# Optimization experiments

Hardware: AMD Instinct MI355X
Metric: run time of the kernel (lower is better)

Reference implementation:

```python
import jax, jax.numpy as jnp
import numpy as np

N, E = 2048, 8192            # n_vertex, n_edge
HV, HE, MV, ME, P, Q = 256, 128, 256, 256, 3, 3
NEG = 1e6                    # PhysChem mask bias: veb = (vew - 1) * 1e6


def _leaky_relu(x, slope=0.01):
    return jnp.where(x >= 0, x, slope * x)


def setup_inputs() -> dict:
    key = jax.random.key(0)
    ks = jax.random.split(key, 12)
    # random graph: each edge has two distinct endpoints
    src = jax.random.randint(ks[0], (E,), 0, N)
    dst = (src + 1 + jax.random.randint(ks[1], (E,), 0, N - 1)) % N
    vew1 = jax.nn.one_hot(src, N, dtype=jnp.float32).T  # [N, E]
    vew2 = jax.nn.one_hot(dst, N, dtype=jnp.float32).T  # [N, E]
    veb1 = (vew1 - 1.0) * NEG
    veb2 = (vew2 - 1.0) * NEG
    s = lambda k, sh, fan: jax.random.normal(k, sh, jnp.float32) / np.sqrt(fan)
    return {
        "hv_ftr": jax.random.normal(ks[2], (N, HV), jnp.float32),
        "he_ftr": jax.random.normal(ks[3], (E, HE), jnp.float32),
        "p_ftr": jax.random.normal(ks[4], (N, P), jnp.float32),
        "q_ftr": jax.random.normal(ks[5], (N, Q), jnp.float32),
        "vew1": vew1, "vew2": vew2, "veb1": veb1, "veb2": veb2,
        "attend_w": s(ks[6], (HV, MV), HV),
        "attend_b": jnp.zeros((MV,), jnp.float32),
        "align_w": s(ks[7], (P + Q + HE, 1), P + Q + HE),
        "align_b": jnp.zeros((1,), jnp.float32),
        "link_w": s(ks[8], (HV + P + Q + HV, ME), HV + P + Q + HV),
        "link_b": jnp.zeros((ME,), jnp.float32),
    }


def reference(hv_ftr, he_ftr, p_ftr, q_ftr, vew1, vew2, veb1, veb2,
              attend_w, attend_b, align_w, align_b, link_w, link_b):
    vew_u = jnp.concatenate([vew1, vew2], axis=1)   # [N, 2E]
    vew_v = jnp.concatenate([vew2, vew1], axis=1)   # [N, 2E]
    veb_v = jnp.concatenate([veb2, veb1], axis=1)   # [N, 2E]

    hv_u = vew_u.T @ hv_ftr                          # [2E, HV]
    hv_v = vew_v.T @ hv_ftr                          # [2E, HV]
    p_uv = vew_v.T @ p_ftr - vew_u.T @ p_ftr         # [2E, P]
    q_uv = vew_v.T @ q_ftr - vew_u.T @ q_ftr         # [2E, Q]
    he2 = jnp.concatenate([he_ftr, he_ftr], axis=0)  # [2E, HE]

    attend = _leaky_relu(hv_v @ attend_w + attend_b)               # [2E, MV]
    align = jnp.concatenate([p_uv, q_uv, he2], axis=1) @ align_w + align_b  # [2E, 1]
    # vew_v @ diag(align) == vew_v * align broadcast over columns
    align_mat = vew_v * align[:, 0][None, :] + veb_v               # [N, 2E]
    soft = jax.nn.softmax(align_mat, axis=-1)
    mv_ftr = jax.nn.elu(soft @ attend)                             # [N, MV]

    me_in = jnp.concatenate([hv_u, p_uv, q_uv, hv_v], axis=1)      # [2E, 2HV+P+Q]
    me_ftr = _leaky_relu(me_in @ link_w + link_b)                  # [2E, ME]
    return (mv_ftr, me_ftr)
```

## Files before the change

### kernel.cpp

```cpp
#include <hip/hip_runtime.h>
#include <math.h>

#define N_V  2048
#define N_E  8192

#define NE4            (N_V * (N_E / 4))
#define SCAN_ITER      8
#define SCAN_BPM       (NE4 / (256 * SCAN_ITER))

static __device__ __forceinline__ float leaky(float x) {
    return x >= 0.f ? x : 0.01f * x;
}

static __device__ __forceinline__ void fma4(float4& c, float a, const float4& b) {
    c.x = fmaf(a, b.x, c.x);
    c.y = fmaf(a, b.y, c.y);
    c.z = fmaf(a, b.z, c.z);
    c.w = fmaf(a, b.w, c.w);
}

__global__ __launch_bounds__(256) void k_scan(const float4* __restrict__ vew1,
                                              const float4* __restrict__ vew2,
                                              int* __restrict__ src,
                                              int* __restrict__ dst)
{
    const int  bm     = blockIdx.x & (SCAN_BPM - 1);
    const bool second = blockIdx.x >= SCAN_BPM;
    const float4* __restrict__ p = second ? vew2 : vew1;
    int* __restrict__ arr        = second ? dst : src;

    const int base = bm * (256 * SCAN_ITER) + threadIdx.x;

    float4 v[SCAN_ITER];
#pragma unroll
    for (int k = 0; k < SCAN_ITER; ++k) v[k] = p[base + k * 256];

#pragma unroll
    for (int k = 0; k < SCAN_ITER; ++k) {
        const float4 q = v[k];
        if (q.x != 0.f || q.y != 0.f || q.z != 0.f || q.w != 0.f) {
            const int i  = base + k * 256;
            const int n  = i >> 11;
            const int e4 = (i & 2047) << 2;
            if (q.x != 0.f) arr[e4 + 0] = n;
            if (q.y != 0.f) arr[e4 + 1] = n;
            if (q.z != 0.f) arr[e4 + 2] = n;
            if (q.w != 0.f) arr[e4 + 3] = n;
        }
    }
}

__global__ __launch_bounds__(256) void k_indeg(const int* __restrict__ src,
                                               const int* __restrict__ dst,
                                               int* __restrict__ indeg)
{
    const int e = blockIdx.x * 256 + threadIdx.x;
    atomicAdd(&indeg[src[e]], 1);
    atomicAdd(&indeg[dst[e]], 1);
}

__global__ __launch_bounds__(256, 3) void k_gemm(const float* __restrict__ hv,
                                                 const float* __restrict__ attend_w,
                                                 const float* __restrict__ attend_b,
                                                 const float* __restrict__ link_w,
                                                 const float* __restrict__ link_b,
                                                 const float* __restrict__ p_ftr,
                                                 const float* __restrict__ q_ftr,
                                                 float* __restrict__ X,
                                                 float* __restrict__ Au,
                                                 float* __restrict__ Av,
                                                 float* __restrict__ mv_out)
{
    __shared__ float As[8 * 256];

    const int mat  = blockIdx.y;
    const int row0 = blockIdx.x * 8;
    const int tid  = threadIdx.x;

    {
        const float4* __restrict__ s4 = (const float4*)(hv + row0 * 256);
        float4* d4 = (float4*)As;
        d4[tid]       = s4[tid];
        d4[tid + 256] = s4[tid + 256];
    }
    __syncthreads();

    const int jq = tid & 63;
    const int rl = (tid >> 6) * 2;
    const float* __restrict__ Arow0 = As + rl * 256;
    const float* __restrict__ Arow1 = Arow0 + 256;
    const int r0 = row0 + rl;

    const float* __restrict__ B =
        (mat == 0) ? attend_w : (mat == 1 ? link_w : link_w + 262 * 256);
    const float4* __restrict__ B4 = (const float4*)B;

    float4 acc0 = make_float4(0.f, 0.f, 0.f, 0.f);
    float4 acc1 = make_float4(0.f, 0.f, 0.f, 0.f);

    float4 ba[8], bb[8];
#pragma unroll
    for (int t = 0; t < 8; ++t) ba[t] = B4[t * 64 + jq];

    for (int ks = 0; ks < 256; ks += 16) {
#pragma unroll
        for (int t = 0; t < 8; ++t) bb[t] = B4[(ks + 8 + t) * 64 + jq];
#pragma unroll
        for (int t4 = 0; t4 < 2; ++t4) {
            const float4 a0 = *reinterpret_cast<const float4*>(Arow0 + ks + t4 * 4);
            const float4 a1 = *reinterpret_cast<const float4*>(Arow1 + ks + t4 * 4);
            fma4(acc0, a0.x, ba[t4 * 4 + 0]);
            fma4(acc0, a0.y, ba[t4 * 4 + 1]);
            fma4(acc0, a0.z, ba[t4 * 4 + 2]);
            fma4(acc0, a0.w, ba[t4 * 4 + 3]);
            fma4(acc1, a1.x, ba[t4 * 4 + 0]);
            fma4(acc1, a1.y, ba[t4 * 4 + 1]);
            fma4(acc1, a1.z, ba[t4 * 4 + 2]);
            fma4(acc1, a1.w, ba[t4 * 4 + 3]);
        }
        const int kn = (ks + 16) & 255;
#pragma unroll
        for (int t = 0; t < 8; ++t) ba[t] = B4[(kn + t) * 64 + jq];
#pragma unroll
        for (int t4 = 0; t4 < 2; ++t4) {
            const float4 a0 = *reinterpret_cast<const float4*>(Arow0 + ks + 8 + t4 * 4);
            const float4 a1 = *reinterpret_cast<const float4*>(Arow1 + ks + 8 + t4 * 4);
            fma4(acc0, a0.x, bb[t4 * 4 + 0]);
            fma4(acc0, a0.y, bb[t4 * 4 + 1]);
            fma4(acc0, a0.z, bb[t4 * 4 + 2]);
            fma4(acc0, a0.w, bb[t4 * 4 + 3]);
            fma4(acc1, a1.x, bb[t4 * 4 + 0]);
            fma4(acc1, a1.y, bb[t4 * 4 + 1]);
            fma4(acc1, a1.z, bb[t4 * 4 + 2]);
            fma4(acc1, a1.w, bb[t4 * 4 + 3]);
        }
    }

    if (mat == 0) {
        const float4 bias = *reinterpret_cast<const float4*>(attend_b + jq * 4);
        float4 a[2] = {acc0, acc1};
#pragma unroll
        for (int r = 0; r < 2; ++r) {
            float4 x;
            x.x = leaky(a[r].x + bias.x);
            x.y = leaky(a[r].y + bias.y);
            x.z = leaky(a[r].z + bias.z);
            x.w = leaky(a[r].w + bias.w);
            *reinterpret_cast<float4*>(X + (r0 + r) * 256 + jq * 4) = x;
            float4 m;
            m.x = (x.x > 0.f) ? x.x : expm1f(x.x);
            m.y = (x.y > 0.f) ? x.y : expm1f(x.y);
            m.z = (x.z > 0.f) ? x.z : expm1f(x.z);
            m.w = (x.w > 0.f) ? x.w : expm1f(x.w);
            *reinterpret_cast<float4*>(mv_out + (r0 + r) * 256 + jq * 4) = m;
        }
    } else {
        float4 w6[6];
#pragma unroll
        for (int t = 0; t < 6; ++t)
            w6[t] = *reinterpret_cast<const float4*>(link_w + (256 + t) * 256 + jq * 4);
        float4 lb = make_float4(0.f, 0.f, 0.f, 0.f);
        if (mat == 2) lb = *reinterpret_cast<const float4*>(link_b + jq * 4);
        float4 a[2] = {acc0, acc1};
#pragma unroll
        for (int r = 0; r < 2; ++r) {
            const int row = r0 + r;
            float4 z = make_float4(0.f, 0.f, 0.f, 0.f);
#pragma unroll
            for (int t = 0; t < 3; ++t) {
                fma4(z, p_ftr[row * 3 + t], w6[t]);
                fma4(z, q_ftr[row * 3 + t], w6[3 + t]);
            }
            float4 o;
            if (mat == 1) {
                o.x = a[r].x - z.x; o.y = a[r].y - z.y;
                o.z = a[r].z - z.z; o.w = a[r].w - z.w;
                *reinterpret_cast<float4*>(Au + row * 256 + jq * 4) = o;
            } else {
                o.x = a[r].x + z.x + lb.x; o.y = a[r].y + z.y + lb.y;
                o.z = a[r].z + z.z + lb.z; o.w = a[r].w + z.w + lb.w;
                *reinterpret_cast<float4*>(Av + row * 256 + jq * 4) = o;
            }
        }
    }
}

__global__ __launch_bounds__(256) void k_sumall(const float* __restrict__ X,
                                                const int* __restrict__ indeg,
                                                float* __restrict__ sumAll)
{
    const int j  = threadIdx.x;
    const int m0 = blockIdx.x * 64;
    float s = 0.f;
    for (int m = m0; m < m0 + 64; ++m) {
        s = fmaf((float)indeg[m], X[m * 256 + j], s);
    }
    atomicAdd(&sumAll[j], s);
}

__global__ __launch_bounds__(256) void k_fix(const int* __restrict__ indeg,
                                             const float* __restrict__ sumAll,
                                             float* __restrict__ out)
{
    const int n = blockIdx.x;
    if (indeg[n] != 0) return;
    const float v = sumAll[threadIdx.x] * (1.0f / (2.0f * N_E));
    out[n * 256 + threadIdx.x] = (v > 0.f) ? v : expm1f(v);
}

__global__ __launch_bounds__(256) void k_me(const int* __restrict__ src,
                                            const int* __restrict__ dst,
                                            const float* __restrict__ Au,
                                            const float* __restrict__ Av,
                                            float* __restrict__ out_me)
{
    const int t    = threadIdx.x;
    const int lane = t & 63;
    const int e    = blockIdx.x * 4 + (t >> 6);
    int u, v;
    if (e < N_E) { u = src[e]; v = dst[e]; }
    else         { u = dst[e - N_E]; v = src[e - N_E]; }
    const float4 a = *reinterpret_cast<const float4*>(&Au[u * 256 + lane * 4]);
    const float4 b = *reinterpret_cast<const float4*>(&Av[v * 256 + lane * 4]);
    float4 o;
    o.x = leaky(a.x + b.x);
    o.y = leaky(a.y + b.y);
    o.z = leaky(a.z + b.z);
    o.w = leaky(a.w + b.w);
    *reinterpret_cast<float4*>(&out_me[e * 256 + lane * 4]) = o;
}

extern "C" void kernel_launch(void* const* d_in, const int* in_sizes, int n_in,
                              void* d_out, int out_size, void* d_ws, size_t ws_size,
                              hipStream_t stream) {
    const float* hv       = (const float*)d_in[0];
    const float* p_ftr    = (const float*)d_in[2];
    const float* q_ftr    = (const float*)d_in[3];
    const float* vew1     = (const float*)d_in[4];
    const float* vew2     = (const float*)d_in[5];
    const float* attend_w = (const float*)d_in[8];
    const float* attend_b = (const float*)d_in[9];
    const float* link_w   = (const float*)d_in[12];
    const float* link_b   = (const float*)d_in[13];

    float* out = (float*)d_out;
    float* ws  = (float*)d_ws;

    int*   src    = (int*)ws;
    int*   dst    = src + N_E;
    int*   indeg  = dst + N_E;
    float* sumAll = ws + 18432;
    float* X      = ws + 32768;
    float* Au     = X + N_V * 256;
    float* Av     = Au + N_V * 256;

    hipMemsetAsync(indeg, 0, (N_V + 256) * sizeof(int), stream);

    k_scan<<<2 * SCAN_BPM, 256, 0, stream>>>((const float4*)vew1,
                                             (const float4*)vew2, src, dst);

    k_indeg<<<N_E / 256, 256, 0, stream>>>(src, dst, indeg);

    dim3 g2(N_V / 8, 3);
    k_gemm<<<g2, 256, 0, stream>>>(hv, attend_w, attend_b, link_w, link_b,
                                   p_ftr, q_ftr, X, Au, Av, out);

    k_sumall<<<32, 256, 0, stream>>>(X, indeg, sumAll);

    k_fix<<<N_V, 256, 0, stream>>>(indeg, sumAll, out);

    k_me<<<(2 * N_E) / 4, 256, 0, stream>>>(src, dst, Au, Av, out + N_V * 256);
}
```

Before: 293.5 us.

## Fuse one-hot scan and dense GEMM into one interleaved launch

Merges the incidence-matrix scan kernel and the hv GEMM kernel into a single launch whose blocks are interleaved 8 scan to 3 GEMM. The bandwidth-bound scan of the 128MB one-hot matrices can then overlap with the compute-bound GEMM instead of running serially. The scan also doubles its per-thread work and tests nonzero with integer bit ops instead of float compares. Because the GEMM does not depend on src/dst, reordering it before k_indeg is safe, but the fused kernel now carries the GEMM's register and LDS footprint for scan blocks too.

```diff
diff --git a/kernel.cpp b/kernel.cpp
--- a/kernel.cpp
+++ b/kernel.cpp
@@ -4,9 +4,12 @@
 #define N_V  2048
 #define N_E  8192
 
-#define NE4            (N_V * (N_E / 4))
-#define SCAN_ITER      8
-#define SCAN_BPM       (NE4 / (256 * SCAN_ITER))
+#define NE4          (N_V * (N_E / 4))
+#define SCAN_ITER    16
+#define SCAN_BPM     (NE4 / (256 * SCAN_ITER))
+#define SCAN_BLOCKS  (2 * SCAN_BPM)
+#define GEMM_BLOCKS  768
+#define FUSED_BLOCKS (SCAN_BLOCKS + GEMM_BLOCKS)
 
 static __device__ __forceinline__ float leaky(float x) {
     return x >= 0.f ? x : 0.01f * x;
@@ -19,63 +22,62 @@
     c.w = fmaf(a, b.w, c.w);
 }
 
-__global__ __launch_bounds__(256) void k_scan(const float4* __restrict__ vew1,
-                                              const float4* __restrict__ vew2,
-                                              int* __restrict__ src,
-                                              int* __restrict__ dst)
-{
-    const int  bm     = blockIdx.x & (SCAN_BPM - 1);
-    const bool second = blockIdx.x >= SCAN_BPM;
-    const float4* __restrict__ p = second ? vew2 : vew1;
-    int* __restrict__ arr        = second ? dst : src;
-
-    const int base = bm * (256 * SCAN_ITER) + threadIdx.x;
-
-    float4 v[SCAN_ITER];
-#pragma unroll
-    for (int k = 0; k < SCAN_ITER; ++k) v[k] = p[base + k * 256];
-
-#pragma unroll
-    for (int k = 0; k < SCAN_ITER; ++k) {
-        const float4 q = v[k];
-        if (q.x != 0.f || q.y != 0.f || q.z != 0.f || q.w != 0.f) {
-            const int i  = base + k * 256;
-            const int n  = i >> 11;
-            const int e4 = (i & 2047) << 2;
-            if (q.x != 0.f) arr[e4 + 0] = n;
-            if (q.y != 0.f) arr[e4 + 1] = n;
-            if (q.z != 0.f) arr[e4 + 2] = n;
-            if (q.w != 0.f) arr[e4 + 3] = n;
-        }
-    }
-}
-
-__global__ __launch_bounds__(256) void k_indeg(const int* __restrict__ src,
-                                               const int* __restrict__ dst,
-                                               int* __restrict__ indeg)
-{
-    const int e = blockIdx.x * 256 + threadIdx.x;
-    atomicAdd(&indeg[src[e]], 1);
-    atomicAdd(&indeg[dst[e]], 1);
-}
-
-__global__ __launch_bounds__(256, 3) void k_gemm(const float* __restrict__ hv,
-                                                 const float* __restrict__ attend_w,
-                                                 const float* __restrict__ attend_b,
-                                                 const float* __restrict__ link_w,
-                                                 const float* __restrict__ link_b,
-                                                 const float* __restrict__ p_ftr,
-                                                 const float* __restrict__ q_ftr,
-                                                 float* __restrict__ X,
-                                                 float* __restrict__ Au,
-                                                 float* __restrict__ Av,
-                                                 float* __restrict__ mv_out)
+__global__ __launch_bounds__(256, 3) void k_scan_gemm(
+        const uint4* __restrict__ vew1,
+        const uint4* __restrict__ vew2,
+        int* __restrict__ src,
+        int* __restrict__ dst,
+        const float* __restrict__ hv,
+        const float* __restrict__ attend_w,
+        const float* __restrict__ attend_b,
+        const float* __restrict__ link_w,
+        const float* __restrict__ link_b,
+        const float* __restrict__ p_ftr,
+        const float* __restrict__ q_ftr,
+        float* __restrict__ X,
+        float* __restrict__ Au,
+        float* __restrict__ Av,
+        float* __restrict__ mv_out)
 {
     __shared__ float As[8 * 256];
 
-    const int mat  = blockIdx.y;
-    const int row0 = blockIdx.x * 8;
-    const int tid  = threadIdx.x;
+    const int g   = blockIdx.x;
+    const int per = g / 11;
+    const int rem = g - per * 11;
+    const int tid = threadIdx.x;
+
+    if (rem < 8) {
+        const int  sid    = per * 8 + rem;
+        const bool second = sid >= SCAN_BPM;
+        const int  bm     = sid & (SCAN_BPM - 1);
+        const uint4* __restrict__ p = second ? vew2 : vew1;
+        int* __restrict__ arr       = second ? dst : src;
+
+        const int base = bm * (256 * SCAN_ITER) + tid;
+
+        uint4 v[SCAN_ITER];
+#pragma unroll
+        for (int k = 0; k < SCAN_ITER; ++k) v[k] = p[base + k * 256];
+
+#pragma unroll
+        for (int k = 0; k < SCAN_ITER; ++k) {
+            const uint4 q = v[k];
+            if (q.x | q.y | q.z | q.w) {
+                const int i  = base + k * 256;
+                const int n  = i >> 11;
+                const int e4 = (i & 2047) << 2;
+                if (q.x) arr[e4 + 0] = n;
+                if (q.y) arr[e4 + 1] = n;
+                if (q.z) arr[e4 + 2] = n;
+                if (q.w) arr[e4 + 3] = n;
+            }
+        }
+        return;
+    }
+
+    const int gid  = per * 3 + (rem - 8);
+    const int mat  = gid >> 8;
+    const int row0 = (gid & 255) * 8;
 
     {
         const float4* __restrict__ s4 = (const float4*)(hv + row0 * 256);
@@ -185,6 +187,15 @@
     }
 }
 
+__global__ __launch_bounds__(256) void k_indeg(const int* __restrict__ src,
+                                               const int* __restrict__ dst,
+                                               int* __restrict__ indeg)
+{
+    const int e = blockIdx.x * 256 + threadIdx.x;
+    atomicAdd(&indeg[src[e]], 1);
+    atomicAdd(&indeg[dst[e]], 1);
+}
+
 __global__ __launch_bounds__(256) void k_sumall(const float* __restrict__ X,
                                                 const int* __restrict__ indeg,
                                                 float* __restrict__ sumAll)
@@ -256,15 +267,13 @@
 
     hipMemsetAsync(indeg, 0, (N_V + 256) * sizeof(int), stream);
 
-    k_scan<<<2 * SCAN_BPM, 256, 0, stream>>>((const float4*)vew1,
-                                             (const float4*)vew2, src, dst);
+    k_scan_gemm<<<FUSED_BLOCKS, 256, 0, stream>>>(
+        (const uint4*)vew1, (const uint4*)vew2, src, dst,
+        hv, attend_w, attend_b, link_w, link_b, p_ftr, q_ftr,
+        X, Au, Av, out);
 
     k_indeg<<<N_E / 256, 256, 0, stream>>>(src, dst, indeg);
 
-    dim3 g2(N_V / 8, 3);
-    k_gemm<<<g2, 256, 0, stream>>>(hv, attend_w, attend_b, link_w, link_b,
-                                   p_ftr, q_ftr, X, Au, Av, out);
-
     k_sumall<<<32, 256, 0, stream>>>(X, indeg, sumAll);
 
     k_fix<<<N_V, 256, 0, stream>>>(indeg, sumAll, out);
```

Result: no change. 289.3 us (-1.4%).
